# Optimization experiments

Hardware: AMD Instinct MI355X
Metric: run time of the kernel (lower is better)

Reference implementation:

```python
import jax, jax.numpy as jnp
import numpy as np


def setup_inputs() -> dict:
    key = jax.random.key(0)
    kx, kw = jax.random.split(key)
    x = jax.random.normal(kx, (32, 256, 56, 56), dtype=jnp.float32)
    weight = jax.random.uniform(kw, (256, 256, 3, 3), dtype=jnp.float32) * 0.001
    return {"x": x, "weight": weight}


def reference(x, weight):
    # --- binarize activations with straight-through estimator ---
    # forward value = sign(x); gradient flows through clamp(x, -1, 1)
    clipped_x = jnp.clip(x, -1.0, 1.0)
    bx = jax.lax.stop_gradient(jnp.sign(x) - clipped_x) + clipped_x

    # --- binarize weights (per-output-channel mean-centered, scaled sign) ---
    w = weight
    # subtract per-output-channel mean over (in_c, kh, kw)
    bw = w - jnp.mean(w.reshape(w.shape[0], -1), axis=-1)[:, None, None, None]
    # per-output-channel scaling factor = mean |bw| (detached)
    scale = jnp.mean(jnp.abs(bw), axis=(1, 2, 3), keepdims=True)
    scale = jax.lax.stop_gradient(scale)
    clipped_w = jnp.clip(bw, -1.0, 1.0)
    binary_w = jax.lax.stop_gradient(scale * jnp.sign(bw) - clipped_w) + clipped_w

    # --- conv2d, NCHW / OIHW, stride 1, padding 1 ---
    y = jax.lax.conv_general_dilated(
        bx, binary_w,
        window_strides=(1, 1),
        padding=((1, 1), (1, 1)),
        dimension_numbers=("NCHW", "OIHW", "NCHW"),
    )
    return y
```

## Files before the change

### kernel.cpp

```cpp
#include <hip/hip_runtime.h>
#include <cstdint>
#include <cstddef>

#define N_ 32
#define C_ 256
#define H_ 56
#define W_ 56

typedef int v4i __attribute__((ext_vector_type(4)));
typedef uint32_t __attribute__((address_space(1))) glb_u32;
typedef uint32_t __attribute__((address_space(3))) lds_u32;

static constexpr size_t SX_BYTES = (size_t)N_ * 58 * 68 * 256;
static constexpr size_t WB_OFF   = SX_BYTES;
static constexpr size_t WB_BYTES = 36ull * 16 * 64 * 16;
static constexpr size_t SC_OFF   = WB_OFF + WB_BYTES;

__global__ __launch_bounds__(256) void pack_x(const float* __restrict__ x,
                                              char* __restrict__ sx) {
    int tid = threadIdx.x;
    int n   = blockIdx.y;
    v4i z = {0, 0, 0, 0};

    if (blockIdx.x >= 49) {
        if (blockIdx.x == 49) {
            for (int i = tid; i < 2 * 58 * 16; i += 256) {
                int r   = i / (58 * 16);
                int rem = i - r * (58 * 16);
                char* base = sx + ((size_t)n * 58 + (size_t)r * 57) * (68 * 256);
                *(v4i*)(base + (size_t)rem * 16) = z;
            }
        } else {
            for (int i = tid; i < 56 * 32; i += 256) {
                int r = 1 + (i >> 5);
                int c = i & 31;
                int wpos = (c >> 4) * 57, ch = c & 15;
                *(v4i*)(sx + (((size_t)n * 58 + r) * 68 + wpos) * 256 + ch * 16) = z;
            }
        }
        return;
    }

    __shared__ float tile[64 * 65];
    __shared__ char  ob[64 * 256];
    int hw0 = blockIdx.x * 64;

    int c16 = tid >> 4, hw4 = tid & 15;
    int hwl2 = tid >> 2, cq  = tid & 3;

    for (int cb = 0; cb < 4; ++cb) {
        const float* xb = x + ((size_t)n * C_ + cb * 64) * 3136 + hw0;
#pragma unroll
        for (int j = 0; j < 4; ++j) {
            int cloc = j * 16 + c16;
            float4 v = *(const float4*)(xb + (size_t)cloc * 3136 + hw4 * 4);
            tile[cloc * 65 + hw4 * 4 + 0] = v.x;
            tile[cloc * 65 + hw4 * 4 + 1] = v.y;
            tile[cloc * 65 + hw4 * 4 + 2] = v.z;
            tile[cloc * 65 + hw4 * 4 + 3] = v.w;
        }
        __syncthreads();
        int words[4];
#pragma unroll
        for (int g = 0; g < 4; ++g) {
            int word = 0;
#pragma unroll
            for (int b = 0; b < 4; ++b) {
                float v = tile[(cq * 16 + g * 4 + b) * 65 + hwl2];
                int s = (v > 0.0f) - (v < 0.0f);
                word |= (s & 0xff) << (8 * b);
            }
            words[g] = word;
        }
        v4i o4 = {words[0], words[1], words[2], words[3]};
        int ch   = cb * 4 + cq;
        int slot = (ch + hwl2) & 15;
        *(v4i*)(ob + hwl2 * 256 + slot * 16) = o4;
        __syncthreads();
    }

#pragma unroll
    for (int j = 0; j < 4; ++j) {
        int i = tid + j * 256;
        int hwl3 = i >> 4, ch = i & 15;
        v4i v = *(const v4i*)(ob + hwl3 * 256 + ((ch + hwl3) & 15) * 16);
        int hw = hw0 + hwl3;
        int h = hw / 56, w = hw - h * 56;
        int slot = (ch + (w + 1)) & 15;
        *(v4i*)(sx + (((size_t)n * 58 + h + 1) * 68 + (w + 1)) * 256 + slot * 16) = v;
    }
}

__global__ __launch_bounds__(256) void pack_w(const float* __restrict__ wt,
                                              char* __restrict__ wB,
                                              float* __restrict__ scaleg) {
    __shared__ double red[256];
    int o = blockIdx.x, tid = threadIdx.x;
    const float* wo = wt + (size_t)o * 2304;

    double s = 0;
    for (int j = tid; j < 2304; j += 256) s += (double)wo[j];
    red[tid] = s;
    __syncthreads();
    for (int k = 128; k > 0; k >>= 1) {
        if (tid < k) red[tid] += red[tid + k];
        __syncthreads();
    }
    double mean = red[0] / 2304.0;
    __syncthreads();

    double s2 = 0;
    for (int j = tid; j < 2304; j += 256) s2 += fabs((double)wo[j] - mean);
    red[tid] = s2;
    __syncthreads();
    for (int k = 128; k > 0; k >>= 1) {
        if (tid < k) red[tid] += red[tid + k];
        __syncthreads();
    }
    if (tid == 0) scaleg[o] = (float)(red[0] / 2304.0);

    if (tid < 144) {
        int kiter = tid >> 2, q = tid & 3;
        int tap = kiter >> 2, cb = kiter & 3;
        int kh = tap / 3, kw = tap - kh * 3;
        int words[4];
        for (int g = 0; g < 4; ++g) {
            int word = 0;
            for (int b = 0; b < 4; ++b) {
                int c = cb * 64 + q * 16 + g * 4 + b;
                double v = (double)wo[c * 9 + kh * 3 + kw];
                int sg = (v > mean) - (v < mean);
                word |= (sg & 0xff) << (8 * b);
            }
            words[g] = word;
        }
        v4i pk = {words[0], words[1], words[2], words[3]};
        *(v4i*)(wB + (((size_t)kiter * 16 + (o >> 4)) * 64 + q * 16 + (o & 15)) * 16) = pk;
    }
}

__device__ __forceinline__ void stage_chunk(const char* src, char* xs, int i) {
    int pos = i >> 4;
    int row = (pos * 1130) >> 16;
    int w   = pos - row * 58;
    const char* g = src + (((size_t)(row * 68 + w)) << 8) + ((size_t)(i & 15) << 4);
    char* l = xs + (size_t)i * 16;
    __builtin_amdgcn_global_load_lds((const glb_u32*)g, (lds_u32*)l, 16, 0, 0);
}

__global__ __launch_bounds__(512, 2) void conv_mfma(const char* __restrict__ sx,
                                                    const v4i* __restrict__ wB,
                                                    const float* __restrict__ scaleg,
                                                    float* __restrict__ out) {
    __shared__ char xs[6 * 58 * 256];
    int tid = threadIdx.x;
    int wave = tid >> 6, lane = tid & 63;
    int hq = blockIdx.x, n = blockIdx.y;
    int h0 = hq * 4;

    const char* src = sx + ((size_t)n * 58 + h0) * (68 * 256);
#pragma unroll
    for (int it = 0; it < 10; ++it) stage_chunk(src, xs, tid + it * 512);
    if (tid < 448) stage_chunk(src, xs, tid + 5120);

    int lm = lane & 15, q = lane >> 4;
    int og = wave & 3, mg = wave >> 2;
    int kstart = __builtin_amdgcn_readfirstlane((9 * wave) >> 1);

    int posb[7], slotb[7];
#pragma unroll
    for (int mf = 0; mf < 7; ++mf) {
        int m = mg * 112 + mf * 16 + lm;
        int r = m / 56;
        int wof = m - r * 56;
        posb[mf]  = r * 58 + wof;
        slotb[mf] = q + wof;
    }

    v4i acc[7][4];
#pragma unroll
    for (int mf = 0; mf < 7; ++mf)
#pragma unroll
        for (int of = 0; of < 4; ++of) { v4i z = {0, 0, 0, 0}; acc[mf][of] = z; }

    const v4i* wBw = wB + (size_t)(og * 4) * 64 + lane;

    __syncthreads();

    v4i bA[4], bB[4], aA[7], aB[7];

    auto loadB = [&](int k, v4i* b) {
#pragma unroll
        for (int of = 0; of < 4; ++of) b[of] = wBw[(size_t)k * 1024 + of * 64];
    };
    auto loadA = [&](int k, v4i* a) {
        int tap = k >> 2, cb = k & 3;
        int dh = (tap * 11) >> 5;
        int dw = tap - dh * 3;
        int pofs = dh * 58 + dw;
        int sofs = cb * 4 + dw;
#pragma unroll
        for (int mf = 0; mf < 7; ++mf) {
            int pos  = posb[mf] + pofs;
            int slot = (slotb[mf] + sofs) & 15;
            a[mf] = *(const v4i*)(xs + ((size_t)pos << 8) + ((size_t)slot << 4));
        }
    };
    auto wrap = [&](int t) { int k = kstart + t; return k >= 36 ? k - 36 : k; };

    loadB(kstart, bA);
    loadA(kstart, aA);

    for (int t2 = 0; t2 < 18; ++t2) {
        int ta = 2 * t2;
        {
            int kb = wrap(ta + 1);
            loadB(kb, bB);
            loadA(kb, aB);
        }
        __builtin_amdgcn_s_setprio(1);
#pragma unroll
        for (int mf = 0; mf < 7; ++mf)
#pragma unroll
            for (int of = 0; of < 4; ++of)
                acc[mf][of] = __builtin_amdgcn_mfma_i32_16x16x64_i8(
                    aA[mf], bA[of], acc[mf][of], 0, 0, 0);
        __builtin_amdgcn_s_setprio(0);
        if (t2 < 17) {
            int kc = wrap(ta + 2);
            loadB(kc, bA);
            loadA(kc, aA);
        }
        __builtin_amdgcn_s_setprio(1);
#pragma unroll
        for (int mf = 0; mf < 7; ++mf)
#pragma unroll
            for (int of = 0; of < 4; ++of)
                acc[mf][of] = __builtin_amdgcn_mfma_i32_16x16x64_i8(
                    aB[mf], bB[of], acc[mf][of], 0, 0, 0);
        __builtin_amdgcn_s_setprio(0);
    }

#pragma unroll
    for (int of = 0; of < 4; ++of) {
        int o = og * 64 + of * 16 + lm;
        float s = scaleg[o];
#pragma unroll
        for (int mf = 0; mf < 7; ++mf) {
            int m  = mg * 112 + mf * 16 + q * 4;
            int r  = m / 56;
            int wb = m - r * 56;
            float* ob = out + ((size_t)(n * C_ + o) * H_ + h0 + r) * W_ + wb;
            float4 v = {s * (float)acc[mf][of].x, s * (float)acc[mf][of].y,
                        s * (float)acc[mf][of].z, s * (float)acc[mf][of].w};
            *(float4*)ob = v;
        }
    }
}

extern "C" void kernel_launch(void* const* d_in, const int* in_sizes, int n_in,
                              void* d_out, int out_size, void* d_ws, size_t ws_size,
                              hipStream_t stream) {
    const float* x   = (const float*)d_in[0];
    const float* wgt = (const float*)d_in[1];
    float* out = (float*)d_out;
    char* ws = (char*)d_ws;

    char*  sx = ws;
    char*  wb = ws + WB_OFF;
    float* sg = (float*)(ws + SC_OFF);

    pack_x<<<dim3(51, N_), dim3(256), 0, stream>>>(x, sx);
    pack_w<<<dim3(256), dim3(256), 0, stream>>>(wgt, wb, sg);
    conv_mfma<<<dim3(14, N_), dim3(512), 0, stream>>>(sx, (const v4i*)wb, sg, out);
}
```

Measured before the change: 251.8 us.

## Pack activations via register byte-permute transpose; triple-buffer weight loads

The activation packer now reads 16 channels per thread directly from global memory, computes sign bytes with bit tricks, and transposes them in registers with byte-permute instructions. This drops the float LDS tile and two barriers per channel block. The conv main loop moves from double-buffering both A and B to a 3-deep rotating prefetch of weight fragments only. A fragments are now loaded from LDS just in time within each step, which may expose LDS latency in exchange for lower register pressure.

```diff
diff --git a/kernel.cpp b/kernel.cpp
--- a/kernel.cpp
+++ b/kernel.cpp
@@ -15,6 +15,10 @@
 static constexpr size_t WB_OFF   = SX_BYTES;
 static constexpr size_t WB_BYTES = 36ull * 16 * 64 * 16;
 static constexpr size_t SC_OFF   = WB_OFF + WB_BYTES;
+
+__device__ __forceinline__ uint32_t sgnw(uint32_t u) {
+    return (u & 0x7fffffffu) ? (((uint32_t)(((int)u) >> 31) | 1u) & 0xffu) : 0u;
+}
 
 __global__ __launch_bounds__(256) void pack_x(const float* __restrict__ x,
                                               char* __restrict__ sx) {
@@ -41,52 +45,65 @@
         return;
     }
 
-    __shared__ float tile[64 * 65];
-    __shared__ char  ob[64 * 256];
+    __shared__ char ob[64 * 256];
     int hw0 = blockIdx.x * 64;
 
-    int c16 = tid >> 4, hw4 = tid & 15;
-    int hwl2 = tid >> 2, cq  = tid & 3;
-
-    for (int cb = 0; cb < 4; ++cb) {
-        const float* xb = x + ((size_t)n * C_ + cb * 64) * 3136 + hw0;
-#pragma unroll
-        for (int j = 0; j < 4; ++j) {
-            int cloc = j * 16 + c16;
-            float4 v = *(const float4*)(xb + (size_t)cloc * 3136 + hw4 * 4);
-            tile[cloc * 65 + hw4 * 4 + 0] = v.x;
-            tile[cloc * 65 + hw4 * 4 + 1] = v.y;
-            tile[cloc * 65 + hw4 * 4 + 2] = v.z;
-            tile[cloc * 65 + hw4 * 4 + 3] = v.w;
-        }
-        __syncthreads();
-        int words[4];
-#pragma unroll
-        for (int g = 0; g < 4; ++g) {
-            int word = 0;
-#pragma unroll
-            for (int b = 0; b < 4; ++b) {
-                float v = tile[(cq * 16 + g * 4 + b) * 65 + hwl2];
-                int s = (v > 0.0f) - (v < 0.0f);
-                word |= (s & 0xff) << (8 * b);
-            }
-            words[g] = word;
-        }
-        v4i o4 = {words[0], words[1], words[2], words[3]};
-        int ch   = cb * 4 + cq;
-        int slot = (ch + hwl2) & 15;
-        *(v4i*)(ob + hwl2 * 256 + slot * 16) = o4;
-        __syncthreads();
-    }
+    int ch  = tid >> 4;
+    int hw4 = tid & 15;
+
+    const float* xb = x + ((size_t)n * C_ + ch * 16) * 3136 + hw0 + hw4 * 4;
+
+    uint32_t t[4][4];
+#pragma unroll
+    for (int p = 0; p < 4; ++p) {
+        uint32_t w0, w1, w2, w3;
+        {
+            float4 v = *(const float4*)(xb + (size_t)(4 * p + 0) * 3136);
+            w0 = sgnw(__float_as_uint(v.x)) | (sgnw(__float_as_uint(v.y)) << 8) |
+                 (sgnw(__float_as_uint(v.z)) << 16) | (sgnw(__float_as_uint(v.w)) << 24);
+        }
+        {
+            float4 v = *(const float4*)(xb + (size_t)(4 * p + 1) * 3136);
+            w1 = sgnw(__float_as_uint(v.x)) | (sgnw(__float_as_uint(v.y)) << 8) |
+                 (sgnw(__float_as_uint(v.z)) << 16) | (sgnw(__float_as_uint(v.w)) << 24);
+        }
+        {
+            float4 v = *(const float4*)(xb + (size_t)(4 * p + 2) * 3136);
+            w2 = sgnw(__float_as_uint(v.x)) | (sgnw(__float_as_uint(v.y)) << 8) |
+                 (sgnw(__float_as_uint(v.z)) << 16) | (sgnw(__float_as_uint(v.w)) << 24);
+        }
+        {
+            float4 v = *(const float4*)(xb + (size_t)(4 * p + 3) * 3136);
+            w3 = sgnw(__float_as_uint(v.x)) | (sgnw(__float_as_uint(v.y)) << 8) |
+                 (sgnw(__float_as_uint(v.z)) << 16) | (sgnw(__float_as_uint(v.w)) << 24);
+        }
+        uint32_t lo01 = __builtin_amdgcn_perm(w1, w0, 0x05010400u);
+        uint32_t hi01 = __builtin_amdgcn_perm(w1, w0, 0x07030602u);
+        uint32_t lo23 = __builtin_amdgcn_perm(w3, w2, 0x05010400u);
+        uint32_t hi23 = __builtin_amdgcn_perm(w3, w2, 0x07030602u);
+        t[p][0] = __builtin_amdgcn_perm(lo23, lo01, 0x05040100u);
+        t[p][1] = __builtin_amdgcn_perm(lo23, lo01, 0x07060302u);
+        t[p][2] = __builtin_amdgcn_perm(hi23, hi01, 0x05040100u);
+        t[p][3] = __builtin_amdgcn_perm(hi23, hi01, 0x07060302u);
+    }
+
+#pragma unroll
+    for (int h = 0; h < 4; ++h) {
+        int row  = hw4 * 4 + h;
+        int slot = (ch + row) & 15;
+        v4i c4 = {(int)t[0][h], (int)t[1][h], (int)t[2][h], (int)t[3][h]};
+        *(v4i*)(ob + row * 256 + slot * 16) = c4;
+    }
+    __syncthreads();
 
 #pragma unroll
     for (int j = 0; j < 4; ++j) {
         int i = tid + j * 256;
-        int hwl3 = i >> 4, ch = i & 15;
-        v4i v = *(const v4i*)(ob + hwl3 * 256 + ((ch + hwl3) & 15) * 16);
+        int hwl3 = i >> 4, cc = i & 15;
+        v4i v = *(const v4i*)(ob + hwl3 * 256 + ((cc + hwl3) & 15) * 16);
         int hw = hw0 + hwl3;
         int h = hw / 56, w = hw - h * 56;
-        int slot = (ch + (w + 1)) & 15;
+        int slot = (cc + (w + 1)) & 15;
         *(v4i*)(sx + (((size_t)n * 58 + h + 1) * 68 + (w + 1)) * 256 + slot * 16) = v;
     }
 }
@@ -185,60 +202,49 @@
 
     const v4i* wBw = wB + (size_t)(og * 4) * 64 + lane;
 
-    __syncthreads();
-
-    v4i bA[4], bB[4], aA[7], aB[7];
-
-    auto loadB = [&](int k, v4i* b) {
+    auto wrap = [&](int t) { int k = kstart + t; return k >= 36 ? k - 36 : k; };
+    auto loadB = [&](int k, v4i (&b)[4]) {
 #pragma unroll
         for (int of = 0; of < 4; ++of) b[of] = wBw[(size_t)k * 1024 + of * 64];
     };
-    auto loadA = [&](int k, v4i* a) {
+
+    __syncthreads();
+
+    v4i bR0[4], bR1[4], bR2[4];
+    loadB(wrap(0), bR0);
+    loadB(wrap(1), bR1);
+    loadB(wrap(2), bR2);
+
+    auto step = [&](v4i (&bReg)[4], int t) {
+        int k = wrap(t);
         int tap = k >> 2, cb = k & 3;
         int dh = (tap * 11) >> 5;
         int dw = tap - dh * 3;
         int pofs = dh * 58 + dw;
         int sofs = cb * 4 + dw;
+        v4i a[7];
 #pragma unroll
         for (int mf = 0; mf < 7; ++mf) {
             int pos  = posb[mf] + pofs;
             int slot = (slotb[mf] + sofs) & 15;
             a[mf] = *(const v4i*)(xs + ((size_t)pos << 8) + ((size_t)slot << 4));
         }
-    };
-    auto wrap = [&](int t) { int k = kstart + t; return k >= 36 ? k - 36 : k; };
-
-    loadB(kstart, bA);
-    loadA(kstart, aA);
-
-    for (int t2 = 0; t2 < 18; ++t2) {
-        int ta = 2 * t2;
-        {
-            int kb = wrap(ta + 1);
-            loadB(kb, bB);
-            loadA(kb, aB);
-        }
         __builtin_amdgcn_s_setprio(1);
 #pragma unroll
         for (int mf = 0; mf < 7; ++mf)
 #pragma unroll
             for (int of = 0; of < 4; ++of)
                 acc[mf][of] = __builtin_amdgcn_mfma_i32_16x16x64_i8(
-                    aA[mf], bA[of], acc[mf][of], 0, 0, 0);
+                    a[mf], bReg[of], acc[mf][of], 0, 0, 0);
         __builtin_amdgcn_s_setprio(0);
-        if (t2 < 17) {
-            int kc = wrap(ta + 2);
-            loadB(kc, bA);
-            loadA(kc, aA);
-        }
-        __builtin_amdgcn_s_setprio(1);
-#pragma unroll
-        for (int mf = 0; mf < 7; ++mf)
-#pragma unroll
-            for (int of = 0; of < 4; ++of)
-                acc[mf][of] = __builtin_amdgcn_mfma_i32_16x16x64_i8(
-                    aB[mf], bB[of], acc[mf][of], 0, 0, 0);
-        __builtin_amdgcn_s_setprio(0);
+        loadB(wrap(t + 3), bReg);
+    };
+
+    for (int t3 = 0; t3 < 12; ++t3) {
+        int t = t3 * 3;
+        step(bR0, t);
+        step(bR1, t + 1);
+        step(bR2, t + 2);
     }
 
 #pragma unroll
```

Result: no change. 251.9 us (+0.1%).
